# Optimization experiments

Measured on AMD Instinct MI355X. Metric: run time of the kernel, lower is better.

Reference implementation:

```python
import jax, jax.numpy as jnp
import numpy as np

D_MODEL = 1024
NUM_HEADS = 16


def setup_inputs() -> dict:
    key = jax.random.key(0)
    ks = jax.random.split(key, 5)
    std = 1.0 / np.sqrt(D_MODEL)
    def w(k):
        return jnp.clip(jax.random.normal(k, (D_MODEL, D_MODEL), dtype=jnp.float32) * std, -3.0, 3.0)
    return {
        "x": jax.random.normal(ks[0], (4, 2048, D_MODEL), dtype=jnp.float32),
        "Wq": w(ks[1]),
        "Wk": w(ks[2]),
        "Wv": w(ks[3]),
        "Wo": w(ks[4]),
    }


def _mha(x, Wq, Wk, Wv, Wo):
    B, S, D = x.shape
    H = NUM_HEADS
    hd = D // H
    # Linear: y = x @ W.T (weights stored [d_out, d_in])
    def proj(W):
        y = jnp.einsum('bsd,ed->bse', x, W)
        return y.reshape(B, S, H, hd).transpose(0, 2, 1, 3)  # b h s d
    q, k, v = proj(Wq), proj(Wk), proj(Wv)
    scores = jnp.einsum('bhqd,bhkd->bhqk', q, k) / np.sqrt(hd)
    causal = jnp.tril(jnp.ones((S, S), dtype=bool))
    scores = jnp.where(causal, scores, -jnp.inf)
    attn = jax.nn.softmax(scores, axis=-1)
    a = jnp.einsum('bhqk,bhkd->bhqd', attn, v)
    a = a.transpose(0, 2, 1, 3).reshape(B, S, D)
    return jnp.einsum('bsd,ed->bse', a, Wo)


def reference(x, Wq, Wk, Wv, Wo):
    return _mha(x, Wq, Wk, Wv, Wo)
```

## Files before the change

### kernel.cpp

```cpp
#include <hip/hip_runtime.h>
#include <hip/hip_bf16.h>
#include <cstdint>
#include <cstddef>


typedef short bf16x8 __attribute__((ext_vector_type(8)));
typedef float f32x4 __attribute__((ext_vector_type(4)));
typedef unsigned int u32x2 __attribute__((ext_vector_type(2)));

__device__ __forceinline__ short f2bf(float f) {
    union { float f; uint32_t u; } c; c.f = f;
    uint32_t r = c.u + 0x7fffu + ((c.u >> 16) & 1u);
    return (short)(r >> 16);
}

__device__ __forceinline__ unsigned cvt_pk_bf16(float lo, float hi) {
    unsigned r;
    asm("v_cvt_pk_bf16_f32 %0, %1, %2" : "=v"(r) : "v"(lo), "v"(hi));
    return r;
}

#define GLOAD_LDS16(g, l) __builtin_amdgcn_global_load_lds( \
    (const __attribute__((address_space(1))) void*)(g),     \
    (__attribute__((address_space(3))) void*)(l), 16, 0, 0)

#define SWZ_RD(base, r, cb) (*(const bf16x8*)((const char*)(base) + (size_t)(r) * 128 + ((cb) ^ (((r) & 7) << 4))))

__global__ __launch_bounds__(256) void convert_kernel(const float* __restrict__ src,
                                                      short* __restrict__ dst) {
    int i = blockIdx.x * 256 + threadIdx.x;
    const float4* s = (const float4*)src + (size_t)i * 2;
    float4 v0 = s[0], v1 = s[1];
    bf16x8 o;
    o[0] = f2bf(v0.x); o[1] = f2bf(v0.y); o[2] = f2bf(v0.z); o[3] = f2bf(v0.w);
    o[4] = f2bf(v1.x); o[5] = f2bf(v1.y); o[6] = f2bf(v1.z); o[7] = f2bf(v1.w);
    *((bf16x8*)dst + i) = o;
}

__global__ __launch_bounds__(256) void convert_w4(const float* __restrict__ w0,
                                                  const float* __restrict__ w1,
                                                  const float* __restrict__ w2,
                                                  const float* __restrict__ w3,
                                                  short* __restrict__ dst) {
    int id = blockIdx.x;
    const float* s = (id < 512) ? w0 : (id < 1024) ? w1 : (id < 1536) ? w2 : w3;
    int i = (id & 511) * 256 + threadIdx.x;
    const float4* sp = (const float4*)s + (size_t)i * 2;
    float4 v0 = sp[0], v1 = sp[1];
    bf16x8 o;
    o[0] = f2bf(v0.x); o[1] = f2bf(v0.y); o[2] = f2bf(v0.z); o[3] = f2bf(v0.w);
    o[4] = f2bf(v1.x); o[5] = f2bf(v1.y); o[6] = f2bf(v1.z); o[7] = f2bf(v1.w);
    *((bf16x8*)(dst + (size_t)(id >> 9) * 1024 * 1024) + i) = o;
}

template<bool OUT_F32>
__device__ __forceinline__ void gemm_body(const short* __restrict__ A,
                                          const short* __restrict__ Bw,
                                          void* __restrict__ Outp,
                                          float escale) {
    __shared__ __align__(16) short As[128 * 64];
    __shared__ __align__(16) short Bs[128 * 64];
    const int tid = threadIdx.x;
    const int lane = tid & 63, w = tid >> 6;
    const int wr = w >> 1, wc = w & 1;
    const int l15 = lane & 15, l4 = lane >> 4;
    const int lin = blockIdx.y * 8 + blockIdx.x;
    const int eff = (lin & 7) * 64 + (lin >> 3);
    const size_t m0 = (size_t)(eff >> 3) * 128;
    const size_t n0 = (size_t)(eff & 7) * 128;

    int srow[4], scol[4];
    #pragma unroll
    for (int i = 0; i < 4; i++) {
        int c = i * 256 + tid;
        srow[i] = c >> 3;
        scol[i] = ((c & 7) ^ (srow[i] & 7)) * 8;
    }

    f32x4 acc[4][4];
    const f32x4 zf = {0.f, 0.f, 0.f, 0.f};
    #pragma unroll
    for (int i = 0; i < 4; i++)
        #pragma unroll
        for (int j = 0; j < 4; j++) acc[i][j] = zf;

    for (int kt = 0; kt < 16; ++kt) {
        const int k0 = kt * 64;
        #pragma unroll
        for (int i = 0; i < 4; i++) {
            GLOAD_LDS16(A  + (m0 + srow[i]) * 1024 + k0 + scol[i], &As[(i * 256 + (w << 6)) * 8]);
            GLOAD_LDS16(Bw + (n0 + srow[i]) * 1024 + k0 + scol[i], &Bs[(i * 256 + (w << 6)) * 8]);
        }
        __syncthreads();

        bf16x8 af[4][2], bfr[4][2];
        #pragma unroll
        for (int mi = 0; mi < 4; mi++) {
            int r = wr * 64 + mi * 16 + l15;
            af[mi][0] = SWZ_RD(As, r, l4 * 16);
            af[mi][1] = SWZ_RD(As, r, 64 + l4 * 16);
        }
        #pragma unroll
        for (int ni = 0; ni < 4; ni++) {
            int r = wc * 64 + ni * 16 + l15;
            bfr[ni][0] = SWZ_RD(Bs, r, l4 * 16);
            bfr[ni][1] = SWZ_RD(Bs, r, 64 + l4 * 16);
        }
        #pragma unroll
        for (int mi = 0; mi < 4; mi++)
            #pragma unroll
            for (int ni = 0; ni < 4; ni++) {
                acc[mi][ni] = __builtin_amdgcn_mfma_f32_16x16x32_bf16(af[mi][0], bfr[ni][0], acc[mi][ni], 0, 0, 0);
                acc[mi][ni] = __builtin_amdgcn_mfma_f32_16x16x32_bf16(af[mi][1], bfr[ni][1], acc[mi][ni], 0, 0, 0);
            }
        __syncthreads();
    }

    #pragma unroll
    for (int mi = 0; mi < 4; mi++) {
        #pragma unroll
        for (int ni = 0; ni < 4; ni++) {
            size_t row = m0 + wr * 64 + mi * 16 + (l4 << 2);
            size_t col = n0 + wc * 64 + ni * 16 + l15;
            #pragma unroll
            for (int j = 0; j < 4; j++) {
                float v = acc[mi][ni][j] * escale;
                if (OUT_F32) ((float*)Outp)[(row + j) * 1024 + col] = v;
                else         ((short*)Outp)[(row + j) * 1024 + col] = f2bf(v);
            }
        }
    }
}

__global__ __launch_bounds__(256) void gemm_qkv(const short* __restrict__ xb,
                                                const short* __restrict__ Wq,
                                                const short* __restrict__ Wk,
                                                const short* __restrict__ Wv,
                                                short* __restrict__ Q,
                                                short* __restrict__ K,
                                                short* __restrict__ V) {
    const short* Bw = (blockIdx.z == 0) ? Wq : (blockIdx.z == 1) ? Wk : Wv;
    short* Out      = (blockIdx.z == 0) ? Q  : (blockIdx.z == 1) ? K  : V;
    float sc = (blockIdx.z == 0) ? 0.18033688011112042f : 1.0f;
    gemm_body<false>(xb, Bw, Out, sc);
}

__global__ __launch_bounds__(256) void gemm_out(const short* __restrict__ Aw,
                                                const short* __restrict__ Wo,
                                                float* __restrict__ Out) {
    gemm_body<true>(Aw, Wo, Out, 1.0f);
}

__global__ __launch_bounds__(256) void transpose_v(const short* __restrict__ Vw,
                                                   short* __restrict__ Vt) {
    __shared__ short T[64][72];
    const int tid = threadIdx.x;
    const int s0 = blockIdx.x * 64;
    const int bh = blockIdx.y, b = bh >> 4, h = bh & 15;
    const int r = tid >> 2, c = tid & 3;
    const size_t srow = (size_t)(b * 2048 + s0 + r) * 1024 + h * 64 + c * 16;
    *(bf16x8*)&T[r][c * 16]     = *(const bf16x8*)&Vw[srow];
    *(bf16x8*)&T[r][c * 16 + 8] = *(const bf16x8*)&Vw[srow + 8];
    __syncthreads();
    short tmp[16];
    #pragma unroll
    for (int i = 0; i < 16; i++) tmp[i] = T[c * 16 + i][r];
    bf16x8 o0, o1;
    #pragma unroll
    for (int i = 0; i < 8; i++) { o0[i] = tmp[i]; o1[i] = tmp[8 + i]; }
    size_t orow = (size_t)(bh * 64 + r) * 2048 + s0 + c * 16;
    *(bf16x8*)&Vt[orow] = o0;
    *(bf16x8*)&Vt[orow + 8] = o1;
}

__global__ __launch_bounds__(512, 4) void attn_kernel(const short* __restrict__ Q,
                                                      const short* __restrict__ K,
                                                      const short* __restrict__ Vt,
                                                      short* __restrict__ Aout) {
    __shared__ __align__(16) short K_lds[2][64 * 64];
    __shared__ __align__(16) short V_lds[2][64 * 64];
    __shared__ __align__(16) short P_lds[8][16][72];
    const int tid = threadIdx.x;
    const int lane = tid & 63, w = tid >> 6;
    const int l15 = lane & 15, l4 = lane >> 4;
    const int bh = blockIdx.x, b = bh >> 4, h = bh & 15;
    const int y = blockIdx.y;
    const int qblk = (y < 4) ? (7 - y) : (y - 4);
    const int qw0 = qblk * 256 + w * 32;
    const short* Qg = Q + (size_t)b * 2048 * 1024 + h * 64;
    const short* Kg = K + (size_t)b * 2048 * 1024 + h * 64;
    const short* Vg = Vt + (size_t)bh * 64 * 2048;

    const int srow = (lane >> 3);
    const int scol = ((lane & 7) ^ srow) * 8;

    bf16x8 qfr[2][2];
    #pragma unroll
    for (int qf = 0; qf < 2; qf++)
        #pragma unroll
        for (int ks = 0; ks < 2; ks++)
            qfr[qf][ks] = *(const bf16x8*)&Qg[(size_t)(qw0 + qf * 16 + l15) * 1024 + ks * 32 + l4 * 8];

    const f32x4 zf = {0.f, 0.f, 0.f, 0.f};
    f32x4 oacc[4][2];
    float l_s[2] = {0.f, 0.f};
    #pragma unroll
    for (int df = 0; df < 4; df++)
        #pragma unroll
        for (int qf = 0; qf < 2; qf++) oacc[df][qf] = zf;

    const int lim = 4 * qblk + 3;

#define KV_RD(base, r, cb) (*(const bf16x8*)((const char*)(base) + (r) * 128 + ((cb) ^ (((r) & 7) << 4))))

    GLOAD_LDS16(Kg + (size_t)(w * 8 + srow) * 1024 + scol, &K_lds[0][w * 512]);
    GLOAD_LDS16(Vg + (size_t)(w * 8 + srow) * 2048 + scol, &V_lds[0][w * 512]);
    __syncthreads();

    int buf = 0;
    for (int t = 0; t <= lim; ++t) {
        const int kv0 = t * 64;
        if (t < lim) {
            const int nv0 = kv0 + 64;
            GLOAD_LDS16(Kg + (size_t)(nv0 + w * 8 + srow) * 1024 + scol, &K_lds[buf ^ 1][w * 512]);
            GLOAD_LDS16(Vg + (size_t)(w * 8 + srow) * 2048 + nv0 + scol, &V_lds[buf ^ 1][w * 512]);
        }

        const int lim_w = (qw0 + 31) >> 6;
        if (t <= lim_w) {
            const short* Kb = K_lds[buf];
            const short* Vb = V_lds[buf];

            f32x4 sacc[4][2];
            #pragma unroll
            for (int kvf = 0; kvf < 4; kvf++)
                #pragma unroll
                for (int qf = 0; qf < 2; qf++) sacc[kvf][qf] = zf;
            __builtin_amdgcn_s_setprio(1);
            #pragma unroll
            for (int kvf = 0; kvf < 4; kvf++) {
                bf16x8 kf0 = KV_RD(Kb, kvf * 16 + l15, l4 * 16);
                bf16x8 kf1 = KV_RD(Kb, kvf * 16 + l15, 64 + l4 * 16);
                #pragma unroll
                for (int qf = 0; qf < 2; qf++) {
                    sacc[kvf][qf] = __builtin_amdgcn_mfma_f32_16x16x32_bf16(kf0, qfr[qf][0], sacc[kvf][qf], 0, 0, 0);
                    sacc[kvf][qf] = __builtin_amdgcn_mfma_f32_16x16x32_bf16(kf1, qfr[qf][1], sacc[kvf][qf], 0, 0, 0);
                }
            }
            __builtin_amdgcn_s_setprio(0);

            if (t == lim_w) {
                #pragma unroll
                for (int kvf = 0; kvf < 4; kvf++)
                    #pragma unroll
                    for (int qf = 0; qf < 2; qf++)
                        #pragma unroll
                        for (int j = 0; j < 4; j++) {
                            int kvg = kv0 + kvf * 16 + l4 * 4 + j;
                            int qg  = qw0 + qf * 16 + l15;
                            if (kvg > qg) sacc[kvf][qf][j] = -1e30f;
                        }
            }

            #pragma unroll
            for (int qf = 0; qf < 2; qf++) {
                float rk[4];
                #pragma unroll
                for (int kvf = 0; kvf < 4; kvf++) {
                    float p0 = __builtin_amdgcn_exp2f(sacc[kvf][qf][0]);
                    float p1 = __builtin_amdgcn_exp2f(sacc[kvf][qf][1]);
                    float p2 = __builtin_amdgcn_exp2f(sacc[kvf][qf][2]);
                    float p3 = __builtin_amdgcn_exp2f(sacc[kvf][qf][3]);
                    sacc[kvf][qf][0] = p0; sacc[kvf][qf][1] = p1;
                    sacc[kvf][qf][2] = p2; sacc[kvf][qf][3] = p3;
                    rk[kvf] = (p0 + p1) + (p2 + p3);
                }
                l_s[qf] += (rk[0] + rk[1]) + (rk[2] + rk[3]);
                #pragma unroll
                for (int kvf = 0; kvf < 4; kvf++) {
                    u32x2 pr;
                    pr[0] = cvt_pk_bf16(sacc[kvf][qf][0], sacc[kvf][qf][1]);
                    pr[1] = cvt_pk_bf16(sacc[kvf][qf][2], sacc[kvf][qf][3]);
                    *(u32x2*)&P_lds[w][l15][kvf * 16 + l4 * 4] = pr;
                }
                asm volatile("s_waitcnt lgkmcnt(0)" ::: "memory");
                __builtin_amdgcn_sched_barrier(0);

                bf16x8 pf0 = *(const bf16x8*)&P_lds[w][l15][l4 * 8];
                bf16x8 pf1 = *(const bf16x8*)&P_lds[w][l15][32 + l4 * 8];

                __builtin_amdgcn_s_setprio(1);
                #pragma unroll
                for (int df = 0; df < 4; df++) {
                    bf16x8 v0 = KV_RD(Vb, df * 16 + l15, l4 * 16);
                    bf16x8 v1 = KV_RD(Vb, df * 16 + l15, 64 + l4 * 16);
                    oacc[df][qf] = __builtin_amdgcn_mfma_f32_16x16x32_bf16(v0, pf0, oacc[df][qf], 0, 0, 0);
                    oacc[df][qf] = __builtin_amdgcn_mfma_f32_16x16x32_bf16(v1, pf1, oacc[df][qf], 0, 0, 0);
                }
                __builtin_amdgcn_s_setprio(0);
            }
        }
        __syncthreads();
        buf ^= 1;
    }

    float rl[2];
    #pragma unroll
    for (int qf = 0; qf < 2; qf++) {
        float l = l_s[qf];
        l += __shfl_xor(l, 16);
        l += __shfl_xor(l, 32);
        rl[qf] = 1.f / l;
    }
    #pragma unroll
    for (int qf = 0; qf < 2; qf++) {
        #pragma unroll
        for (int df = 0; df < 4; df++) {
            u32x2 pr;
            pr[0] = cvt_pk_bf16(oacc[df][qf][0] * rl[qf], oacc[df][qf][1] * rl[qf]);
            pr[1] = cvt_pk_bf16(oacc[df][qf][2] * rl[qf], oacc[df][qf][3] * rl[qf]);
            *(u32x2*)&P_lds[w][l15][df * 16 + l4 * 4] = pr;
        }
        asm volatile("s_waitcnt lgkmcnt(0)" ::: "memory");
        __builtin_amdgcn_sched_barrier(0);
        const int r = lane >> 2, cq = lane & 3;
        size_t orow = (size_t)(b * 2048 + qw0 + qf * 16 + r) * 1024 + h * 64;
        *(bf16x8*)&Aout[orow + cq * 8]       = *(const bf16x8*)&P_lds[w][r][cq * 8];
        *(bf16x8*)&Aout[orow + (cq + 4) * 8] = *(const bf16x8*)&P_lds[w][r][(cq + 4) * 8];
        asm volatile("s_waitcnt lgkmcnt(0)" ::: "memory");
        __builtin_amdgcn_sched_barrier(0);
    }
#undef KV_RD
}

extern "C" void kernel_launch(void* const* d_in, const int* in_sizes, int n_in,
                              void* d_out, int out_size, void* d_ws, size_t ws_size,
                              hipStream_t stream) {
    const float* x  = (const float*)d_in[0];
    const float* Wq = (const float*)d_in[1];
    const float* Wk = (const float*)d_in[2];
    const float* Wv = (const float*)d_in[3];
    const float* Wo = (const float*)d_in[4];
    float* out = (float*)d_out;

    const size_t NX = (size_t)8192 * 1024;
    const size_t NW = (size_t)1024 * 1024;
    short* xb  = (short*)d_ws;
    short* Wqb = xb  + NX;
    short* Wkb = Wqb + NW;
    short* Wvb = Wkb + NW;
    short* Wob = Wvb + NW;
    short* Qw  = Wob + NW;
    short* Kw  = Qw + NX;
    short* Vw  = (short*)d_out;
    short* Vt  = Vw + NX;
    short* Aw  = xb;

    hipLaunchKernelGGL(convert_kernel, dim3(NX / 2048), dim3(256), 0, stream, x, xb);
    hipLaunchKernelGGL(convert_w4, dim3(2048), dim3(256), 0, stream, Wq, Wk, Wv, Wo, Wqb);

    hipLaunchKernelGGL(gemm_qkv, dim3(8, 64, 3), dim3(256), 0, stream, xb, Wqb, Wkb, Wvb, Qw, Kw, Vw);
    hipLaunchKernelGGL(transpose_v, dim3(32, 64), dim3(256), 0, stream, Vw, Vt);
    hipLaunchKernelGGL(attn_kernel, dim3(64, 8), dim3(512), 0, stream, Qw, Kw, Vt, Aw);
    hipLaunchKernelGGL(gemm_out, dim3(8, 64), dim3(256), 0, stream, Aw, Wob, out);
}
```

Before: 163.1 us.

## Fuse V transpose into QKV GEMM epilogue, merge conversions, batch PV MFMAs

The two fp32-to-bf16 conversion kernels become a single launch, and the V projection GEMM now writes its output directly in the transposed [b,h,d,s] layout, so the separate transpose kernel is removed. In attention, P for both 16-row q fragments is staged together in a larger LDS buffer, so each V fragment read from LDS feeds two MFMAs and the wait/barrier count per KV step drops. The final output staging is batched the same way. The costs are strided 8-byte scattered stores in the V epilogue and doubled per-wave P LDS, which could hurt occupancy.

```diff
diff --git a/kernel.cpp b/kernel.cpp
--- a/kernel.cpp
+++ b/kernel.cpp
@@ -26,38 +26,40 @@
 
 #define SWZ_RD(base, r, cb) (*(const bf16x8*)((const char*)(base) + (size_t)(r) * 128 + ((cb) ^ (((r) & 7) << 4))))
 
-__global__ __launch_bounds__(256) void convert_kernel(const float* __restrict__ src,
-                                                      short* __restrict__ dst) {
-    int i = blockIdx.x * 256 + threadIdx.x;
-    const float4* s = (const float4*)src + (size_t)i * 2;
-    float4 v0 = s[0], v1 = s[1];
-    bf16x8 o;
-    o[0] = f2bf(v0.x); o[1] = f2bf(v0.y); o[2] = f2bf(v0.z); o[3] = f2bf(v0.w);
-    o[4] = f2bf(v1.x); o[5] = f2bf(v1.y); o[6] = f2bf(v1.z); o[7] = f2bf(v1.w);
-    *((bf16x8*)dst + i) = o;
-}
-
-__global__ __launch_bounds__(256) void convert_w4(const float* __restrict__ w0,
-                                                  const float* __restrict__ w1,
-                                                  const float* __restrict__ w2,
-                                                  const float* __restrict__ w3,
-                                                  short* __restrict__ dst) {
+__global__ __launch_bounds__(256) void convert_all(const float* __restrict__ x,
+                                                   const float* __restrict__ w0,
+                                                   const float* __restrict__ w1,
+                                                   const float* __restrict__ w2,
+                                                   const float* __restrict__ w3,
+                                                   short* __restrict__ dst) {
+    const size_t NX = (size_t)8192 * 1024;
+    const size_t NW = (size_t)1024 * 1024;
     int id = blockIdx.x;
-    const float* s = (id < 512) ? w0 : (id < 1024) ? w1 : (id < 1536) ? w2 : w3;
-    int i = (id & 511) * 256 + threadIdx.x;
-    const float4* sp = (const float4*)s + (size_t)i * 2;
+    const float* src;
+    short* d;
+    int i;
+    if (id < 4096) {
+        src = x; d = dst; i = id * 256 + threadIdx.x;
+    } else {
+        int idw = id - 4096;
+        int wsel = idw >> 9;
+        src = (wsel == 0) ? w0 : (wsel == 1) ? w1 : (wsel == 2) ? w2 : w3;
+        d = dst + NX + (size_t)wsel * NW;
+        i = (idw & 511) * 256 + threadIdx.x;
+    }
+    const float4* sp = (const float4*)src + (size_t)i * 2;
     float4 v0 = sp[0], v1 = sp[1];
     bf16x8 o;
     o[0] = f2bf(v0.x); o[1] = f2bf(v0.y); o[2] = f2bf(v0.z); o[3] = f2bf(v0.w);
     o[4] = f2bf(v1.x); o[5] = f2bf(v1.y); o[6] = f2bf(v1.z); o[7] = f2bf(v1.w);
-    *((bf16x8*)(dst + (size_t)(id >> 9) * 1024 * 1024) + i) = o;
+    *((bf16x8*)d + i) = o;
 }
 
 template<bool OUT_F32>
 __device__ __forceinline__ void gemm_body(const short* __restrict__ A,
                                           const short* __restrict__ Bw,
                                           void* __restrict__ Outp,
-                                          float escale) {
+                                          float escale, bool vtmode) {
     __shared__ __align__(16) short As[128 * 64];
     __shared__ __align__(16) short Bs[128 * 64];
     const int tid = threadIdx.x;
@@ -116,17 +118,33 @@
         __syncthreads();
     }
 
-    #pragma unroll
-    for (int mi = 0; mi < 4; mi++) {
-        #pragma unroll
-        for (int ni = 0; ni < 4; ni++) {
-            size_t row = m0 + wr * 64 + mi * 16 + (l4 << 2);
-            size_t col = n0 + wc * 64 + ni * 16 + l15;
-            #pragma unroll
-            for (int j = 0; j < 4; j++) {
-                float v = acc[mi][ni][j] * escale;
-                if (OUT_F32) ((float*)Outp)[(row + j) * 1024 + col] = v;
-                else         ((short*)Outp)[(row + j) * 1024 + col] = f2bf(v);
+    if (vtmode) {
+        #pragma unroll
+        for (int mi = 0; mi < 4; mi++) {
+            #pragma unroll
+            for (int ni = 0; ni < 4; ni++) {
+                size_t s   = m0 + wr * 64 + mi * 16 + (l4 << 2);
+                size_t col = n0 + wc * 64 + ni * 16 + l15;
+                size_t bb = s >> 11, sl = s & 2047;
+                u32x2 pr;
+                pr[0] = cvt_pk_bf16(acc[mi][ni][0], acc[mi][ni][1]);
+                pr[1] = cvt_pk_bf16(acc[mi][ni][2], acc[mi][ni][3]);
+                *(u32x2*)&((short*)Outp)[(bb * 1024 + col) * 2048 + sl] = pr;
+            }
+        }
+    } else {
+        #pragma unroll
+        for (int mi = 0; mi < 4; mi++) {
+            #pragma unroll
+            for (int ni = 0; ni < 4; ni++) {
+                size_t row = m0 + wr * 64 + mi * 16 + (l4 << 2);
+                size_t col = n0 + wc * 64 + ni * 16 + l15;
+                #pragma unroll
+                for (int j = 0; j < 4; j++) {
+                    float v = acc[mi][ni][j] * escale;
+                    if (OUT_F32) ((float*)Outp)[(row + j) * 1024 + col] = v;
+                    else         ((short*)Outp)[(row + j) * 1024 + col] = f2bf(v);
+                }
             }
         }
     }
@@ -138,39 +156,17 @@
                                                 const short* __restrict__ Wv,
                                                 short* __restrict__ Q,
                                                 short* __restrict__ K,
-                                                short* __restrict__ V) {
+                                                short* __restrict__ Vt) {
     const short* Bw = (blockIdx.z == 0) ? Wq : (blockIdx.z == 1) ? Wk : Wv;
-    short* Out      = (blockIdx.z == 0) ? Q  : (blockIdx.z == 1) ? K  : V;
+    short* Out      = (blockIdx.z == 0) ? Q  : (blockIdx.z == 1) ? K  : Vt;
     float sc = (blockIdx.z == 0) ? 0.18033688011112042f : 1.0f;
-    gemm_body<false>(xb, Bw, Out, sc);
+    gemm_body<false>(xb, Bw, Out, sc, blockIdx.z == 2);
 }
 
 __global__ __launch_bounds__(256) void gemm_out(const short* __restrict__ Aw,
                                                 const short* __restrict__ Wo,
                                                 float* __restrict__ Out) {
-    gemm_body<true>(Aw, Wo, Out, 1.0f);
-}
-
-__global__ __launch_bounds__(256) void transpose_v(const short* __restrict__ Vw,
-                                                   short* __restrict__ Vt) {
-    __shared__ short T[64][72];
-    const int tid = threadIdx.x;
-    const int s0 = blockIdx.x * 64;
-    const int bh = blockIdx.y, b = bh >> 4, h = bh & 15;
-    const int r = tid >> 2, c = tid & 3;
-    const size_t srow = (size_t)(b * 2048 + s0 + r) * 1024 + h * 64 + c * 16;
-    *(bf16x8*)&T[r][c * 16]     = *(const bf16x8*)&Vw[srow];
-    *(bf16x8*)&T[r][c * 16 + 8] = *(const bf16x8*)&Vw[srow + 8];
-    __syncthreads();
-    short tmp[16];
-    #pragma unroll
-    for (int i = 0; i < 16; i++) tmp[i] = T[c * 16 + i][r];
-    bf16x8 o0, o1;
-    #pragma unroll
-    for (int i = 0; i < 8; i++) { o0[i] = tmp[i]; o1[i] = tmp[8 + i]; }
-    size_t orow = (size_t)(bh * 64 + r) * 2048 + s0 + c * 16;
-    *(bf16x8*)&Vt[orow] = o0;
-    *(bf16x8*)&Vt[orow + 8] = o1;
+    gemm_body<true>(Aw, Wo, Out, 1.0f, false);
 }
 
 __global__ __launch_bounds__(512, 4) void attn_kernel(const short* __restrict__ Q,
@@ -179,7 +175,7 @@
                                                       short* __restrict__ Aout) {
     __shared__ __align__(16) short K_lds[2][64 * 64];
     __shared__ __align__(16) short V_lds[2][64 * 64];
-    __shared__ __align__(16) short P_lds[8][16][72];
+    __shared__ __align__(16) short P_lds[8][32][72];
     const int tid = threadIdx.x;
     const int lane = tid & 63, w = tid >> 6;
     const int l15 = lane & 15, l4 = lane >> 4;
@@ -281,24 +277,31 @@
                     u32x2 pr;
                     pr[0] = cvt_pk_bf16(sacc[kvf][qf][0], sacc[kvf][qf][1]);
                     pr[1] = cvt_pk_bf16(sacc[kvf][qf][2], sacc[kvf][qf][3]);
-                    *(u32x2*)&P_lds[w][l15][kvf * 16 + l4 * 4] = pr;
-                }
-                asm volatile("s_waitcnt lgkmcnt(0)" ::: "memory");
-                __builtin_amdgcn_sched_barrier(0);
-
-                bf16x8 pf0 = *(const bf16x8*)&P_lds[w][l15][l4 * 8];
-                bf16x8 pf1 = *(const bf16x8*)&P_lds[w][l15][32 + l4 * 8];
-
-                __builtin_amdgcn_s_setprio(1);
-                #pragma unroll
-                for (int df = 0; df < 4; df++) {
-                    bf16x8 v0 = KV_RD(Vb, df * 16 + l15, l4 * 16);
-                    bf16x8 v1 = KV_RD(Vb, df * 16 + l15, 64 + l4 * 16);
-                    oacc[df][qf] = __builtin_amdgcn_mfma_f32_16x16x32_bf16(v0, pf0, oacc[df][qf], 0, 0, 0);
-                    oacc[df][qf] = __builtin_amdgcn_mfma_f32_16x16x32_bf16(v1, pf1, oacc[df][qf], 0, 0, 0);
-                }
-                __builtin_amdgcn_s_setprio(0);
-            }
+                    *(u32x2*)&P_lds[w][qf * 16 + l15][kvf * 16 + l4 * 4] = pr;
+                }
+            }
+            asm volatile("s_waitcnt lgkmcnt(0)" ::: "memory");
+            __builtin_amdgcn_sched_barrier(0);
+
+            bf16x8 pf[2][2];
+            #pragma unroll
+            for (int qf = 0; qf < 2; qf++)
+                #pragma unroll
+                for (int ks = 0; ks < 2; ks++)
+                    pf[qf][ks] = *(const bf16x8*)&P_lds[w][qf * 16 + l15][ks * 32 + l4 * 8];
+
+            __builtin_amdgcn_s_setprio(1);
+            #pragma unroll
+            for (int df = 0; df < 4; df++) {
+                bf16x8 v0 = KV_RD(Vb, df * 16 + l15, l4 * 16);
+                bf16x8 v1 = KV_RD(Vb, df * 16 + l15, 64 + l4 * 16);
+                #pragma unroll
+                for (int qf = 0; qf < 2; qf++) {
+                    oacc[df][qf] = __builtin_amdgcn_mfma_f32_16x16x32_bf16(v0, pf[qf][0], oacc[df][qf], 0, 0, 0);
+                    oacc[df][qf] = __builtin_amdgcn_mfma_f32_16x16x32_bf16(v1, pf[qf][1], oacc[df][qf], 0, 0, 0);
+                }
+            }
+            __builtin_amdgcn_s_setprio(0);
         }
         __syncthreads();
         buf ^= 1;
@@ -313,22 +316,24 @@
         rl[qf] = 1.f / l;
     }
     #pragma unroll
-    for (int qf = 0; qf < 2; qf++) {
+    for (int qf = 0; qf < 2; qf++)
         #pragma unroll
         for (int df = 0; df < 4; df++) {
             u32x2 pr;
             pr[0] = cvt_pk_bf16(oacc[df][qf][0] * rl[qf], oacc[df][qf][1] * rl[qf]);
             pr[1] = cvt_pk_bf16(oacc[df][qf][2] * rl[qf], oacc[df][qf][3] * rl[qf]);
-            *(u32x2*)&P_lds[w][l15][df * 16 + l4 * 4] = pr;
-        }
-        asm volatile("s_waitcnt lgkmcnt(0)" ::: "memory");
-        __builtin_amdgcn_sched_barrier(0);
+            *(u32x2*)&P_lds[w][qf * 16 + l15][df * 16 + l4 * 4] = pr;
+        }
+    asm volatile("s_waitcnt lgkmcnt(0)" ::: "memory");
+    __builtin_amdgcn_sched_barrier(0);
+    {
         const int r = lane >> 2, cq = lane & 3;
-        size_t orow = (size_t)(b * 2048 + qw0 + qf * 16 + r) * 1024 + h * 64;
-        *(bf16x8*)&Aout[orow + cq * 8]       = *(const bf16x8*)&P_lds[w][r][cq * 8];
-        *(bf16x8*)&Aout[orow + (cq + 4) * 8] = *(const bf16x8*)&P_lds[w][r][(cq + 4) * 8];
-        asm volatile("s_waitcnt lgkmcnt(0)" ::: "memory");
-        __builtin_amdgcn_sched_barrier(0);
+        #pragma unroll
+        for (int qf = 0; qf < 2; qf++) {
+            size_t orow = (size_t)(b * 2048 + qw0 + qf * 16 + r) * 1024 + h * 64;
+            *(bf16x8*)&Aout[orow + cq * 8]       = *(const bf16x8*)&P_lds[w][qf * 16 + r][cq * 8];
+            *(bf16x8*)&Aout[orow + (cq + 4) * 8] = *(const bf16x8*)&P_lds[w][qf * 16 + r][(cq + 4) * 8];
+        }
     }
 #undef KV_RD
 }
@@ -352,15 +357,11 @@
     short* Wob = Wvb + NW;
     short* Qw  = Wob + NW;
     short* Kw  = Qw + NX;
-    short* Vw  = (short*)d_out;
-    short* Vt  = Vw + NX;
+    short* Vt  = (short*)d_out + NX;
     short* Aw  = xb;
 
-    hipLaunchKernelGGL(convert_kernel, dim3(NX / 2048), dim3(256), 0, stream, x, xb);
-    hipLaunchKernelGGL(convert_w4, dim3(2048), dim3(256), 0, stream, Wq, Wk, Wv, Wo, Wqb);
-
-    hipLaunchKernelGGL(gemm_qkv, dim3(8, 64, 3), dim3(256), 0, stream, xb, Wqb, Wkb, Wvb, Qw, Kw, Vw);
-    hipLaunchKernelGGL(transpose_v, dim3(32, 64), dim3(256), 0, stream, Vw, Vt);
+    hipLaunchKernelGGL(convert_all, dim3(6144), dim3(256), 0, stream, x, Wq, Wk, Wv, Wo, xb);
+    hipLaunchKernelGGL(gemm_qkv, dim3(8, 64, 3), dim3(256), 0, stream, xb, Wqb, Wkb, Wvb, Qw, Kw, Vt);
     hipLaunchKernelGGL(attn_kernel, dim3(64, 8), dim3(512), 0, stream, Qw, Kw, Vt, Aw);
     hipLaunchKernelGGL(gemm_out, dim3(8, 64), dim3(256), 0, stream, Aw, Wob, out);
 }
```

Measured after the change: 158.6 us. -2.8%, faster.
